# Performance work log

Hardware: AMD Instinct MI355X
Metric: run time of the kernel (lower is better)

## Reference

```python
import jax, jax.numpy as jnp
import numpy as np

NUM_EDGES = 4000
NODES_PER_EDGE = 25
D_IN = 128
NUM_PROJ = 128
NUM_ANCHORS = 64
EPS = 1e-5


def sparse_sort(src, index):
    """Per-column stable sort of src (N,P), grouped by 1D segment index (N,).
    Mirrors the repo's sparse_sort: min-max normalize to [0,1] then add segment id."""
    fmin = src.min(axis=0, keepdims=True)
    fmax = src.max(axis=0, keepdims=True)
    norm = (src - fmin) / (fmax - fmin + 1e-12) + index[:, None].astype(src.dtype)
    perm = jnp.argsort(norm, axis=0, stable=True)  # (N, P)
    return jnp.take_along_axis(src, perm, axis=0), perm


def setup_inputs() -> dict:
    key = jax.random.key(0)
    k1, k2, k3 = jax.random.split(key, 3)
    n_inc = NUM_EDGES * NODES_PER_EDGE
    X = jax.random.normal(k1, (n_inc, D_IN), dtype=jnp.float32)
    # sorted segment ids, every edge has >=2 members -> double_self_loops is a no-op
    hyperedge_index = jnp.repeat(jnp.arange(NUM_EDGES, dtype=jnp.int32), NODES_PER_EDGE)
    theta_v = jax.random.normal(k2, (NUM_PROJ, D_IN), dtype=jnp.float32)
    # reference anchors: linspace(-1,1,M) replicated over projections (as in __init__)
    ref_anchors = jnp.tile(jnp.linspace(-1.0, 1.0, NUM_ANCHORS, dtype=jnp.float32)[:, None], (1, NUM_PROJ))
    weight = jax.random.normal(k3, (NUM_PROJ, NUM_ANCHORS), dtype=jnp.float32) * 0.1
    return {"X": X, "theta_v": theta_v, "ref_anchors": ref_anchors, "weight": weight,
            "hyperedge_index": hyperedge_index, "num_edges": NUM_EDGES}


def reference(X, theta_v, ref_anchors, weight, hyperedge_index, num_edges):
    P = theta_v.shape[0]
    M = ref_anchors.shape[0]
    dt = X.dtype
    # weight_norm with g=1: rows of v normalized to unit L2
    W = theta_v / jnp.linalg.norm(theta_v, axis=1, keepdims=True)
    Xslices = X @ W.T  # (N, P) slices
    Xslices_sorted, perm = sparse_sort(Xslices, hyperedge_index)
    seg = hyperedge_index[perm[:, 0]]  # segment id per sorted row (N,)
    N = seg.shape[0]
    # per-segment degree, pointer offsets
    D1 = jax.ops.segment_sum(jnp.ones(N, dt), seg, num_segments=num_edges)  # (E,)
    ptr = jnp.concatenate([jnp.zeros(1, dt), jnp.cumsum(D1)])
    D = D1[seg]
    Pofs = ptr[seg]
    R = jnp.arange(N, dtype=dt) + 1.0
    # sample positions: within-segment quantile in (0,1) + segment offset -> globally sorted
    x = (R - Pofs - 1.0) / (D - 1.0) * 0.99999 + EPS + seg.astype(dt)  # (N,)
    edges = jnp.arange(num_edges, dtype=jnp.int32)
    grid = jnp.linspace(0.0, 1.0, M).astype(dt) * 0.99998 + EPS  # (M,)
    xnew = (edges[:, None].astype(dt) + grid[None, :]).reshape(-1)  # (E*M,)
    # interp1d: x/xnew identical across projections -> one searchsorted, broadcast interp
    y = Xslices_sorted.T  # (P, N)
    ind = jnp.clip(jnp.searchsorted(x, xnew), 1, N - 1)  # (E*M,)
    x0, x1 = x[ind - 1], x[ind]
    t = ((xnew - x0) / (x1 - x0))[None, :]  # (1, E*M)
    ynew = y[:, ind - 1] + (y[:, ind] - y[:, ind - 1]) * t  # (P, E*M)
    Xsi = ynew.T  # (E*M, P)
    # reference slices per edge, sorted within segments (identity for sorted anchors)
    seg_anchor = jnp.repeat(edges, M)  # (E*M,)
    Rslices = jnp.tile(ref_anchors, (num_edges, 1))  # (E*M, P)
    _, Rind = sparse_sort(Rslices, seg_anchor)
    emb = Rslices - jnp.take_along_axis(Xsi, Rind, axis=0)  # (E*M, P)
    emb = emb.T.reshape(P, num_edges, M)
    out = (weight[:, None, :] * emb).mean(-1).T  # (E, P)
    return out, edges
```

## Files before the change

kernel.cpp:

```cpp
#include <hip/hip_runtime.h>
#include <math.h>

#define NEDGE 4000
#define NPE   25
#define DIN   128
#define NPROJ 128
#define NANCH 64
#define NROWS (NEDGE*NPE)
#define NBLK  (NROWS/32)

__device__ __forceinline__ float xval_of(int g) {
  int ee = g / NPE;
  int jj = g - ee * NPE;
  float t1 = __fdiv_rn((float)jj, 24.0f);
  float t2 = __fmul_rn(t1, 0.99999f);
  float t3 = __fadd_rn(t2, 1e-5f);
  return __fadd_rn(t3, (float)ee);
}

__global__ __launch_bounds__(128) void k_prep(const float* __restrict__ theta,
                                              float* __restrict__ Wt) {
  int p = threadIdx.x;
  float s = 0.f;
  #pragma unroll 8
  for (int k = 0; k < DIN; ++k) { float t = theta[p*DIN + k]; s = fmaf(t, t, s); }
  float nrm = sqrtf(s);
  for (int k = 0; k < DIN; ++k)
    Wt[k*NPROJ + p] = __fdiv_rn(theta[p*DIN + k], nrm);
}

__global__ __launch_bounds__(256) void k_gemm(const float* __restrict__ X,
                                              const float* __restrict__ Wt,
                                              float* __restrict__ Xs,
                                              float* __restrict__ pmin,
                                              float* __restrict__ pmax) {
  __shared__ float sW[32 * NPROJ];
  __shared__ float sX[32 * DIN];
  const int tid = threadIdx.x;
  const int rbase = blockIdx.x * 32;
  {
    const float4* src = (const float4*)(X + (size_t)rbase * DIN);
    float4* dst = (float4*)sX;
    #pragma unroll
    for (int i = 0; i < 4; ++i) dst[tid + 256*i] = src[tid + 256*i];
  }
  const int cg = tid & 31, rg = tid >> 5;
  const int p0 = cg * 4, r0 = rg * 4;
  float acc[4][4] = {};
  for (int ph = 0; ph < 4; ++ph) {
    __syncthreads();
    {
      const float4* src = (const float4*)(Wt + ph * 32 * NPROJ);
      float4* dst = (float4*)sW;
      #pragma unroll
      for (int i = 0; i < 4; ++i) dst[tid + 256*i] = src[tid + 256*i];
    }
    __syncthreads();
    #pragma unroll
    for (int k0 = 0; k0 < 32; k0 += 4) {
      float4 w[4];
      #pragma unroll
      for (int i = 0; i < 4; ++i) w[i] = *(const float4*)&sW[(k0+i)*NPROJ + p0];
      #pragma unroll
      for (int i = 0; i < 4; ++i) {
        float4 xv = *(const float4*)&sX[(r0+i)*DIN + ph*32 + k0];
        const float xs[4] = {xv.x, xv.y, xv.z, xv.w};
        #pragma unroll
        for (int kk = 0; kk < 4; ++kk) {
          acc[i][0] = fmaf(xs[kk], w[kk].x, acc[i][0]);
          acc[i][1] = fmaf(xs[kk], w[kk].y, acc[i][1]);
          acc[i][2] = fmaf(xs[kk], w[kk].z, acc[i][2]);
          acc[i][3] = fmaf(xs[kk], w[kk].w, acc[i][3]);
        }
      }
    }
  }
  #pragma unroll
  for (int i = 0; i < 4; ++i) {
    float4 st = make_float4(acc[i][0], acc[i][1], acc[i][2], acc[i][3]);
    *(float4*)&Xs[(size_t)(rbase + r0 + i)*NPROJ + p0] = st;
  }
  __syncthreads();
  float* rmn = sX;
  float* rmx = sX + 8*NPROJ;
  #pragma unroll
  for (int c = 0; c < 4; ++c) {
    float mn = fminf(fminf(acc[0][c], acc[1][c]), fminf(acc[2][c], acc[3][c]));
    float mx = fmaxf(fmaxf(acc[0][c], acc[1][c]), fmaxf(acc[2][c], acc[3][c]));
    rmn[rg*NPROJ + p0 + c] = mn;
    rmx[rg*NPROJ + p0 + c] = mx;
  }
  __syncthreads();
  if (tid < NPROJ) {
    float mn = rmn[tid], mx = rmx[tid];
    #pragma unroll
    for (int g2 = 1; g2 < 8; ++g2) {
      mn = fminf(mn, rmn[g2*NPROJ + tid]);
      mx = fmaxf(mx, rmx[g2*NPROJ + tid]);
    }
    pmin[(size_t)blockIdx.x*NPROJ + tid] = mn;
    pmax[(size_t)blockIdx.x*NPROJ + tid] = mx;
  }
}

__global__ __launch_bounds__(256) void k_red1(const float* __restrict__ pmin,
                                              const float* __restrict__ pmax,
                                              float* __restrict__ imn,
                                              float* __restrict__ imx) {
  __shared__ float smn[NPROJ], smx[NPROJ];
  const int tid = threadIdx.x, p = tid & 127, h = tid >> 7;
  const int b = blockIdx.x;
  float mn = INFINITY, mx = -INFINITY;
  for (int s = 125*b + h; s < 125*(b+1); s += 2) {
    mn = fminf(mn, pmin[(size_t)s*NPROJ + p]);
    mx = fmaxf(mx, pmax[(size_t)s*NPROJ + p]);
  }
  if (h == 1) { smn[p] = mn; smx[p] = mx; }
  __syncthreads();
  if (h == 0) {
    imn[b*NPROJ + p] = fminf(mn, smn[p]);
    imx[b*NPROJ + p] = fmaxf(mx, smx[p]);
  }
}

__global__ __launch_bounds__(256) void k_red2(const float* __restrict__ imn,
                                              const float* __restrict__ imx,
                                              float* __restrict__ fmn,
                                              float* __restrict__ fmx) {
  __shared__ float smn[NPROJ], smx[NPROJ];
  const int tid = threadIdx.x, p = tid & 127, h = tid >> 7;
  float mn = INFINITY, mx = -INFINITY;
  for (int s = h; s < 25; s += 2) {
    mn = fminf(mn, imn[s*NPROJ + p]);
    mx = fmaxf(mx, imx[s*NPROJ + p]);
  }
  if (h == 1) { smn[p] = mn; smx[p] = mx; }
  __syncthreads();
  if (h == 0) { fmn[p] = fminf(mn, smn[p]); fmx[p] = fmaxf(mx, smx[p]); }
}

__global__ __launch_bounds__(128) void k_main(const float* __restrict__ Xs,
                                              const float* __restrict__ fmnA,
                                              const float* __restrict__ fmxA,
                                              const float* __restrict__ anchors,
                                              const float* __restrict__ weight,
                                              float* __restrict__ out) {
  __shared__ float svals[NPE * NPROJ];
  __shared__ float sprev[2 * NPROJ];
  __shared__ int   sind[NANCH];
  __shared__ float stt[NANCH];
  const int e = blockIdx.x;
  const int p = threadIdx.x;
  const float ef = (float)e;
  const float fmin = fmnA[p];
  const float denom = __fadd_rn(__fsub_rn(fmxA[p], fmin), 1e-12f);

  float v[NPE];
  unsigned ku[NPE];
  #pragma unroll
  for (int j = 0; j < NPE; ++j) {
    float x = Xs[(size_t)(e*NPE + j)*NPROJ + p];
    v[j] = x;
    ku[j] = __float_as_uint(__fadd_rn(__fdiv_rn(__fsub_rn(x, fmin), denom), ef));
  }
  #pragma unroll
  for (int i = 0; i < NPE; ++i) {
    int cnt = 0;
    #pragma unroll
    for (int j = 0; j < NPE; ++j) {
      if (j == i) continue;
      cnt += (j < i) ? (ku[j] <= ku[i]) : (ku[j] < ku[i]);
    }
    svals[cnt*NPROJ + p] = v[i];
  }
  if (e > 0) {
    const float efp = (float)(e - 1);
    unsigned k1 = 0u, k2 = 0u;
    float v1 = 0.f, v2 = 0.f;
    #pragma unroll
    for (int j = 0; j < NPE; ++j) {
      float x = Xs[(size_t)((e-1)*NPE + j)*NPROJ + p];
      unsigned kk = __float_as_uint(
          __fadd_rn(__fdiv_rn(__fsub_rn(x, fmin), denom), efp));
      if (kk >= k1)      { k2 = k1; v2 = v1; k1 = kk; v1 = x; }
      else if (kk >= k2) { k2 = kk; v2 = x; }
    }
    sprev[p]         = v2;
    sprev[NPROJ + p] = v1;
  }
  __syncthreads();

  if (p < NANCH) {
    const int m = p;
    const float delta = __fdiv_rn(1.0f, 63.0f);
    float g = __fmul_rn((float)m, delta);
    g = __fadd_rn(__fmul_rn(g, 0.99998f), 1e-5f);
    const float xnew = __fadd_rn(ef, g);
    int lo = e*NPE - 1; if (lo < 0) lo = 0;
    const int hi = e*NPE + (NPE - 1);
    int ind = -1;
    for (int j = lo; j <= hi; ++j) {
      float xg = xval_of(j);
      if (ind < 0 && xg >= xnew) ind = j;
    }
    if (ind < 0) ind = hi;
    if (ind < 1) ind = 1;
    float x0 = xval_of(ind - 1);
    float x1 = xval_of(ind);
    stt[m]  = __fdiv_rn(__fsub_rn(xnew, x0), __fsub_rn(x1, x0));
    sind[m] = ind;
  }
  __syncthreads();

  float acc = 0.f;
  const int base = e * NPE;
  for (int m = 0; m < NANCH; ++m) {
    const int ind = sind[m];
    const float t = stt[m];
    const int o1 = ind - base;
    const int o0 = o1 - 1;
    const float y1 = (o1 >= 0) ? svals[o1*NPROJ + p] : sprev[(o1 + 2)*NPROJ + p];
    const float y0 = (o0 >= 0) ? svals[o0*NPROJ + p] : sprev[(o0 + 2)*NPROJ + p];
    const float ynew = __fadd_rn(y0, __fmul_rn(__fsub_rn(y1, y0), t));
    const float emb  = __fsub_rn(anchors[m*NPROJ + p], ynew);
    acc = __fadd_rn(acc, __fmul_rn(weight[p*NANCH + m], emb));
  }
  out[(size_t)e*NPROJ + p] = __fmul_rn(acc, 0.015625f);
  if (p == 0) out[NEDGE*NPROJ + e] = (float)e;
}

extern "C" void kernel_launch(void* const* d_in, const int* in_sizes, int n_in,
                              void* d_out, int out_size, void* d_ws, size_t ws_size,
                              hipStream_t stream) {
  (void)in_sizes; (void)n_in; (void)out_size; (void)ws_size;
  const float* X      = (const float*)d_in[0];
  const float* theta  = (const float*)d_in[1];
  const float* anchor = (const float*)d_in[2];
  const float* weight = (const float*)d_in[3];
  float* out = (float*)d_out;
  float* ws  = (float*)d_ws;

  float* Xs   = ws;
  float* Wt   = Xs   + (size_t)NROWS*NPROJ;
  float* pmin = Wt   + DIN*NPROJ;
  float* pmax = pmin + (size_t)NBLK*NPROJ;
  float* imn  = pmax + (size_t)NBLK*NPROJ;
  float* imx  = imn  + 25*NPROJ;
  float* fmn  = imx  + 25*NPROJ;
  float* fmx  = fmn  + NPROJ;

  k_prep<<<1, 128, 0, stream>>>(theta, Wt);
  k_gemm<<<NBLK, 256, 0, stream>>>(X, Wt, Xs, pmin, pmax);
  k_red1<<<25, 256, 0, stream>>>(pmin, pmax, imn, imx);
  k_red2<<<1, 256, 0, stream>>>(imn, imx, fmn, fmx);
  k_main<<<NEDGE, 128, 0, stream>>>(Xs, fmn, fmx, anchor, weight, out);
}
```

Measured before the change: 228.8 us.

## Split main kernel into in-place sort and interpolation epilogue with interleaved anchor/weight table

The main kernel is split into two launches. The first sorts each edge's rows in place in the workspace. The second reads the already-sorted neighbour rows directly instead of recomputing the previous edge's top two keys, and reads anchors and transposed weights from a table interleaved in the prep kernel, so the weight loads become coalesced. The split removes the redundant per-block sort of the previous segment and the strided weight access. In exchange it adds a full extra write and reread of the 51 MB projection buffer plus one more kernel launch.

```diff
diff --git a/kernel.cpp b/kernel.cpp
--- a/kernel.cpp
+++ b/kernel.cpp
@@ -19,7 +19,10 @@
 }
 
 __global__ __launch_bounds__(128) void k_prep(const float* __restrict__ theta,
-                                              float* __restrict__ Wt) {
+                                              const float* __restrict__ anchors,
+                                              const float* __restrict__ weight,
+                                              float* __restrict__ Wt,
+                                              float* __restrict__ awT) {
   int p = threadIdx.x;
   float s = 0.f;
   #pragma unroll 8
@@ -27,6 +30,11 @@
   float nrm = sqrtf(s);
   for (int k = 0; k < DIN; ++k)
     Wt[k*NPROJ + p] = __fdiv_rn(theta[p*DIN + k], nrm);
+  #pragma unroll
+  for (int m = 0; m < NANCH; ++m) {
+    awT[(2*m    )*NPROJ + p] = anchors[m*NPROJ + p];
+    awT[(2*m + 1)*NPROJ + p] = weight[p*NANCH + m];
+  }
 }
 
 __global__ __launch_bounds__(256) void k_gemm(const float* __restrict__ X,
@@ -139,56 +147,56 @@
   if (h == 0) { fmn[p] = fminf(mn, smn[p]); fmx[p] = fmaxf(mx, smx[p]); }
 }
 
-__global__ __launch_bounds__(128) void k_main(const float* __restrict__ Xs,
+__global__ __launch_bounds__(128) void k_sort(float* Xs,
                                               const float* __restrict__ fmnA,
-                                              const float* __restrict__ fmxA,
-                                              const float* __restrict__ anchors,
-                                              const float* __restrict__ weight,
-                                              float* __restrict__ out) {
+                                              const float* __restrict__ fmxA) {
   __shared__ float svals[NPE * NPROJ];
-  __shared__ float sprev[2 * NPROJ];
+  const int e = blockIdx.x;
+  const int p = threadIdx.x;
+  const float ef = (float)e;
+  const float fmin = fmnA[p];
+  const float denom = __fadd_rn(__fsub_rn(fmxA[p], fmin), 1e-12f);
+
+  float v[NPE];
+  unsigned ku[NPE];
+  #pragma unroll
+  for (int j = 0; j < NPE; ++j) {
+    float x = Xs[(size_t)(e*NPE + j)*NPROJ + p];
+    v[j] = x;
+    ku[j] = __float_as_uint(__fadd_rn(__fdiv_rn(__fsub_rn(x, fmin), denom), ef));
+  }
+  #pragma unroll
+  for (int i = 0; i < NPE; ++i) {
+    int cnt = 0;
+    #pragma unroll
+    for (int j = 0; j < NPE; ++j) {
+      if (j == i) continue;
+      cnt += (j < i) ? (ku[j] <= ku[i]) : (ku[j] < ku[i]);
+    }
+    svals[cnt*NPROJ + p] = v[i];
+  }
+  #pragma unroll
+  for (int j = 0; j < NPE; ++j)
+    Xs[(size_t)(e*NPE + j)*NPROJ + p] = svals[j*NPROJ + p];
+}
+
+__global__ __launch_bounds__(128) void k_epi(const float* __restrict__ Xs,
+                                             const float* __restrict__ awT,
+                                             float* __restrict__ out) {
+  __shared__ float sv[(NPE + 2) * NPROJ];
   __shared__ int   sind[NANCH];
   __shared__ float stt[NANCH];
   const int e = blockIdx.x;
   const int p = threadIdx.x;
   const float ef = (float)e;
-  const float fmin = fmnA[p];
-  const float denom = __fadd_rn(__fsub_rn(fmxA[p], fmin), 1e-12f);
-
-  float v[NPE];
-  unsigned ku[NPE];
-  #pragma unroll
-  for (int j = 0; j < NPE; ++j) {
-    float x = Xs[(size_t)(e*NPE + j)*NPROJ + p];
-    v[j] = x;
-    ku[j] = __float_as_uint(__fadd_rn(__fdiv_rn(__fsub_rn(x, fmin), denom), ef));
-  }
-  #pragma unroll
-  for (int i = 0; i < NPE; ++i) {
-    int cnt = 0;
-    #pragma unroll
-    for (int j = 0; j < NPE; ++j) {
-      if (j == i) continue;
-      cnt += (j < i) ? (ku[j] <= ku[i]) : (ku[j] < ku[i]);
-    }
-    svals[cnt*NPROJ + p] = v[i];
-  }
+
   if (e > 0) {
-    const float efp = (float)(e - 1);
-    unsigned k1 = 0u, k2 = 0u;
-    float v1 = 0.f, v2 = 0.f;
-    #pragma unroll
-    for (int j = 0; j < NPE; ++j) {
-      float x = Xs[(size_t)((e-1)*NPE + j)*NPROJ + p];
-      unsigned kk = __float_as_uint(
-          __fadd_rn(__fdiv_rn(__fsub_rn(x, fmin), denom), efp));
-      if (kk >= k1)      { k2 = k1; v2 = v1; k1 = kk; v1 = x; }
-      else if (kk >= k2) { k2 = kk; v2 = x; }
-    }
-    sprev[p]         = v2;
-    sprev[NPROJ + p] = v1;
-  }
-  __syncthreads();
+    sv[p]         = Xs[(size_t)((e-1)*NPE + 23)*NPROJ + p];
+    sv[NPROJ + p] = Xs[(size_t)((e-1)*NPE + 24)*NPROJ + p];
+  }
+  #pragma unroll
+  for (int j = 0; j < NPE; ++j)
+    sv[(2 + j)*NPROJ + p] = Xs[(size_t)(e*NPE + j)*NPROJ + p];
 
   if (p < NANCH) {
     const int m = p;
@@ -218,12 +226,11 @@
     const int ind = sind[m];
     const float t = stt[m];
     const int o1 = ind - base;
-    const int o0 = o1 - 1;
-    const float y1 = (o1 >= 0) ? svals[o1*NPROJ + p] : sprev[(o1 + 2)*NPROJ + p];
-    const float y0 = (o0 >= 0) ? svals[o0*NPROJ + p] : sprev[(o0 + 2)*NPROJ + p];
+    const float y1 = sv[(o1 + 2)*NPROJ + p];
+    const float y0 = sv[(o1 + 1)*NPROJ + p];
     const float ynew = __fadd_rn(y0, __fmul_rn(__fsub_rn(y1, y0), t));
-    const float emb  = __fsub_rn(anchors[m*NPROJ + p], ynew);
-    acc = __fadd_rn(acc, __fmul_rn(weight[p*NANCH + m], emb));
+    const float emb  = __fsub_rn(awT[(2*m)*NPROJ + p], ynew);
+    acc = __fadd_rn(acc, __fmul_rn(awT[(2*m + 1)*NPROJ + p], emb));
   }
   out[(size_t)e*NPROJ + p] = __fmul_rn(acc, 0.015625f);
   if (p == 0) out[NEDGE*NPROJ + e] = (float)e;
@@ -242,16 +249,18 @@
 
   float* Xs   = ws;
   float* Wt   = Xs   + (size_t)NROWS*NPROJ;
-  float* pmin = Wt   + DIN*NPROJ;
+  float* awT  = Wt   + DIN*NPROJ;
+  float* pmin = awT  + 2*NANCH*NPROJ;
   float* pmax = pmin + (size_t)NBLK*NPROJ;
   float* imn  = pmax + (size_t)NBLK*NPROJ;
   float* imx  = imn  + 25*NPROJ;
   float* fmn  = imx  + 25*NPROJ;
   float* fmx  = fmn  + NPROJ;
 
-  k_prep<<<1, 128, 0, stream>>>(theta, Wt);
+  k_prep<<<1, 128, 0, stream>>>(theta, anchor, weight, Wt, awT);
   k_gemm<<<NBLK, 256, 0, stream>>>(X, Wt, Xs, pmin, pmax);
   k_red1<<<25, 256, 0, stream>>>(pmin, pmax, imn, imx);
   k_red2<<<1, 256, 0, stream>>>(imn, imx, fmn, fmx);
-  k_main<<<NEDGE, 128, 0, stream>>>(Xs, fmn, fmx, anchor, weight, out);
-}
+  k_sort<<<NEDGE, 128, 0, stream>>>(Xs, fmn, fmx);
+  k_epi <<<NEDGE, 128, 0, stream>>>(Xs, awT, out);
+}
```

Measured after the change: 219.3 us. -4.2%, faster.
